# Kernel tuning notes

Hardware: AMD Instinct MI355X
Metric: run time of the kernel (lower is better)

The kernel has to match this reference:

```python
import jax, jax.numpy as jnp
import numpy as np

N, E, F, H, C, G = 100000, 800000, 128, 128, 10, 128
EPS = 1e-5


def setup_inputs() -> dict:
    key = jax.random.key(0)
    ks = jax.random.split(key, 8)
    return {
        "x": jax.random.normal(ks[0], (N, F), jnp.float32),
        "edge_index": jax.random.randint(ks[1], (2, E), 0, N),
        "batch": jnp.sort(jax.random.randint(ks[2], (N,), 0, G)),
        "edge_weight": jax.random.uniform(ks[3], (E,), jnp.float32, 0.1, 1.0),
        "bn_feat_w": jnp.ones((F,), jnp.float32),
        "bn_feat_b": jnp.full((F,), 1e-4, jnp.float32),
        "conv_feat_W": jax.random.normal(ks[4], (F, H), jnp.float32) / np.float32(np.sqrt(F)),
        "conv_feat_b": jnp.zeros((H,), jnp.float32),
        "bns_w": jnp.ones((3, H), jnp.float32),
        "bns_b": jnp.full((3, H), 1e-4, jnp.float32),
        "convs_W": jax.random.normal(ks[5], (3, H, H), jnp.float32) / np.float32(np.sqrt(H)),
        "convs_b": jnp.zeros((3, H), jnp.float32),
        "bn_fc_w": jnp.ones((H,), jnp.float32),
        "bn_fc_b": jnp.full((H,), 1e-4, jnp.float32),
        "lin_fc_W": jax.random.normal(ks[6], (H, H), jnp.float32) / np.float32(np.sqrt(H)),
        "lin_fc_b": jnp.zeros((H,), jnp.float32),
        "bn_hidden_w": jnp.ones((H,), jnp.float32),
        "bn_hidden_b": jnp.full((H,), 1e-4, jnp.float32),
        "lin_class_W": jax.random.normal(ks[7], (H, C), jnp.float32) / np.float32(np.sqrt(H)),
        "lin_class_b": jnp.zeros((C,), jnp.float32),
    }


def _bn(h, w, b):
    # training-mode BatchNorm1d: biased batch stats over dim 0
    mu = h.mean(0)
    var = jnp.mean((h - mu) ** 2, 0)
    return (h - mu) * jax.lax.rsqrt(var + EPS) * w + b


def reference(x, edge_index, batch, edge_weight,
              bn_feat_w, bn_feat_b, conv_feat_W, conv_feat_b,
              bns_w, bns_b, convs_W, convs_b,
              bn_fc_w, bn_fc_b, lin_fc_W, lin_fc_b,
              bn_hidden_w, bn_hidden_b, lin_class_W, lin_class_b):
    n = x.shape[0]
    loops = jnp.arange(n)
    # PyG GCNConv: add self-loops (weight 1) + symmetric normalization, shared by all convs
    row = jnp.concatenate([edge_index[0], loops])
    col = jnp.concatenate([edge_index[1], loops])
    ew = jnp.concatenate([edge_weight, jnp.ones((n,), x.dtype)])
    deg = jax.ops.segment_sum(ew, col, num_segments=n)
    dinv = jnp.where(deg > 0, jax.lax.rsqrt(jnp.maximum(deg, EPS)), 0.0)
    norm = (dinv[row] * ew * dinv[col])[:, None]  # [E+N, 1]

    def conv(h, W, b):
        m = (h @ W)[row] * norm                 # gather + scale per edge
        return jax.ops.segment_sum(m, col, num_segments=n) + b

    h = _bn(x, bn_feat_w, bn_feat_b)
    h = jax.nn.relu(conv(h, conv_feat_W, conv_feat_b))
    h_init = h

    x_list = []
    # branch 1: BN -> Conv -> ReLU chain
    h = h_init
    for i in range(3):
        h = jax.nn.relu(conv(_bn(h, bns_w[i], bns_b[i]), convs_W[i], convs_b[i]))
    x_list.append(h)
    # branch 2: double application of the same BN/Conv per step
    h = h_init
    for i in range(3):
        h_ = jax.nn.relu(conv(_bn(h, bns_w[i], bns_b[i]), convs_W[i], convs_b[i]))
        h = jax.nn.relu(conv(_bn(h_, bns_w[i], bns_b[i]), convs_W[i], convs_b[i]))
    x_list.append(h)
    # branch 3: identical to branch 1 when conv_residual=False
    h = h_init
    for i in range(3):
        h = jax.nn.relu(conv(_bn(h, bns_w[i], bns_b[i]), convs_W[i], convs_b[i]))
    x_list.append(h)
    # branch 4: BN -> ReLU only
    h = h_init
    for i in range(3):
        h = jax.nn.relu(_bn(h, bns_w[i], bns_b[i]))
    x_list.append(h)

    def head(hn):
        g = jax.ops.segment_sum(hn, batch, num_segments=G)  # global_add_pool
        g = jax.nn.relu(_bn(g, bn_fc_w, bn_fc_b) @ lin_fc_W + lin_fc_b)
        g = _bn(g, bn_hidden_w, bn_hidden_b)
        return jax.nn.log_softmax(g @ lin_class_W + lin_class_b, axis=-1)

    return tuple(head(hn) for hn in x_list)
```

## Files before the change

kernel.cpp:

```cpp
#include <hip/hip_runtime.h>

#define N_NODES 100000
#define NPAD    100032
#define NBLK    1563
#define NEDGE   800000
#define NGRP    128
#define NSLOT   32
#define EPS     1e-5f

typedef unsigned int   u32;
typedef unsigned short u16;
typedef short bf16x8 __attribute__((ext_vector_type(8)));
typedef float f32x4  __attribute__((ext_vector_type(4)));

__device__ __forceinline__ float bf2f(u32 u){ return __uint_as_float(u << 16); }
__device__ __forceinline__ u16 f2bf(float f){
  u32 x = __float_as_uint(f);
  x += 0x7fffu + ((x >> 16) & 1u);
  return (u16)(x >> 16);
}

__global__ void k_init(float* deg, int* cnt, int* fill, float* gbuf){
  int i = blockIdx.x * 256 + threadIdx.x;
  if (i < NPAD){ deg[i] = 1.0f; cnt[i] = 0; fill[i] = 0; }
  if (i < 4 * NGRP * 128) gbuf[i] = 0.f;
}

__global__ void k_deg(const int* __restrict__ col, const float* __restrict__ ew,
                      float* __restrict__ deg, int* __restrict__ cnt){
  int e = blockIdx.x * 256 + threadIdx.x;
  if (e < NEDGE){
    int c = col[e];
    atomicAdd(&deg[c], ew[e]);
    atomicAdd(&cnt[c], 1);
  }
}

__global__ void k_dinv(const float* __restrict__ deg, float* __restrict__ dinv, float* __restrict__ srow){
  int i = blockIdx.x * 256 + threadIdx.x;
  if (i < N_NODES){
    float d = deg[i];
    float v = d > 0.f ? rsqrtf(fmaxf(d, EPS)) : 0.f;
    dinv[i] = v; srow[i] = v * v;
  }
}

__global__ __launch_bounds__(256) void k_chunksum(const int* __restrict__ cnt, int* __restrict__ csum){
  int b = blockIdx.x, t = threadIdx.x;
  int s = 0;
  for (int i = t; i < 1024; i += 256){ int idx = b * 1024 + i; if (idx < N_NODES) s += cnt[idx]; }
  __shared__ int red[256];
  red[t] = s; __syncthreads();
  for (int o = 128; o > 0; o >>= 1){ if (t < o) red[t] += red[t + o]; __syncthreads(); }
  if (t == 0) csum[b] = red[0];
}

__global__ __launch_bounds__(128) void k_chunkscan(const int* __restrict__ csum, int* __restrict__ coff,
                                                   int* __restrict__ ptrA){
  int t = threadIdx.x;
  __shared__ int s[128];
  int v = (t < 98) ? csum[t] : 0;
  s[t] = v; __syncthreads();
  for (int o = 1; o < 128; o <<= 1){
    int x = (t >= o) ? s[t - o] : 0;
    __syncthreads(); s[t] += x; __syncthreads();
  }
  if (t < 98) coff[t] = s[t] - v;
  if (t == 0) ptrA[N_NODES] = NEDGE;
}

__global__ __launch_bounds__(256) void k_scan2(const int* __restrict__ cnt, const int* __restrict__ coff,
                                               int* __restrict__ ptrA){
  int b = blockIdx.x, t = threadIdx.x;
  int base = b * 1024 + t * 4;
  int v[4], tot = 0;
  #pragma unroll
  for (int k = 0; k < 4; k++){ int idx = base + k; v[k] = (idx < N_NODES) ? cnt[idx] : 0; tot += v[k]; }
  __shared__ int sc[256];
  sc[t] = tot; __syncthreads();
  for (int o = 1; o < 256; o <<= 1){
    int x = (t >= o) ? sc[t - o] : 0;
    __syncthreads(); sc[t] += x; __syncthreads();
  }
  int off = coff[b] + sc[t] - tot;
  #pragma unroll
  for (int k = 0; k < 4; k++){ int idx = base + k; if (idx < N_NODES) ptrA[idx] = off; off += v[k]; }
}

__global__ void k_fill(const int* __restrict__ row, const int* __restrict__ col,
                       const float* __restrict__ ew, const float* __restrict__ dinv,
                       const int* __restrict__ ptrA, int* __restrict__ fill, int2* __restrict__ adj,
                       float* __restrict__ srow){
  int e = blockIdx.x * 256 + threadIdx.x;
  if (e < NEDGE){
    int r = row[e], c = col[e];
    float w = dinv[r] * ew[e] * dinv[c];
    int pos = ptrA[c] + atomicAdd(&fill[c], 1);
    adj[pos] = make_int2(r, __float_as_int(w));
    atomicAdd(&srow[c], w);
  }
}

__global__ __launch_bounds__(256) void k_bhist(const int* __restrict__ batch, int* __restrict__ bpart){
  __shared__ int loc[128];
  int t = threadIdx.x;
  if (t < 128) loc[t] = 0;
  __syncthreads();
  int i = blockIdx.x * 256 + t;
  if (i < N_NODES) atomicAdd(&loc[batch[i]], 1);
  __syncthreads();
  if (t < 128) bpart[blockIdx.x * 128 + t] = loc[t];
}

__global__ __launch_bounds__(128) void k_bscan(const int* __restrict__ bpart, int* __restrict__ gptr){
  int t = threadIdx.x;
  int v = 0;
  for (int p = 0; p < 391; p++) v += bpart[p * 128 + t];
  __shared__ int s[128];
  s[t] = v; __syncthreads();
  for (int o = 1; o < 128; o <<= 1){
    int x = (t >= o) ? s[t - o] : 0;
    __syncthreads(); s[t] += x; __syncthreads();
  }
  gptr[t + 1] = s[t];
  if (t == 0) gptr[0] = 0;
}

__global__ __launch_bounds__(256) void k_cvtstats(const float* __restrict__ x, u32* __restrict__ dst,
                                                  float* __restrict__ sums_out){
  __shared__ float R[1024];
  int t = threadIdx.x;
  float s0 = 0.f, q0 = 0.f, s1 = 0.f, q1 = 0.f;
  size_t base = (size_t)blockIdx.x * 4096 + t;
  #pragma unroll
  for (int it = 0; it < 16; it++){
    size_t idx = base + (size_t)it * 256;
    if (idx < (size_t)N_NODES * 64){
      float2 v = ((const float2*)x)[idx];
      dst[idx] = (u32)f2bf(v.x) | ((u32)f2bf(v.y) << 16);
      s0 += v.x; q0 += v.x * v.x; s1 += v.y; q1 += v.y * v.y;
    }
  }
  R[t] = s0; R[256 + t] = q0; R[512 + t] = s1; R[768 + t] = q1;
  __syncthreads();
  if (t < 64){
    float S0 = 0.f, Q0 = 0.f, S1 = 0.f, Q1 = 0.f;
    #pragma unroll
    for (int g = 0; g < 4; g++){
      S0 += R[g * 64 + t];       Q0 += R[256 + g * 64 + t];
      S1 += R[512 + g * 64 + t]; Q1 += R[768 + g * 64 + t];
    }
    float* so = sums_out + (blockIdx.x & (NSLOT - 1)) * 256;
    atomicAdd(&so[2 * t], S0);
    atomicAdd(&so[2 * t + 1], S1);
    atomicAdd(&so[128 + 2 * t], Q0);
    atomicAdd(&so[128 + 2 * t + 1], Q1);
  }
}

__device__ __forceinline__ void fold_body(int blk, int t, const float* __restrict__ sums,
    const float* __restrict__ bw, const float* __restrict__ bb,
    const float* __restrict__ W, const float* __restrict__ bias,
    u16* __restrict__ Wh, u16* __restrict__ Wl, float* __restrict__ rb,
    float* scl, float* shf, float* stot, float* rred){
  {
    float s = 0.f;
    #pragma unroll 4
    for (int sl = 0; sl < NSLOT; sl++) s += sums[sl * 256 + t];
    stot[t] = s;
  }
  __syncthreads();
  if (t < 128){
    float mu  = stot[t] * (1.f / N_NODES);
    float var = stot[128 + t] * (1.f / N_NODES) - mu * mu;
    float sc  = bw[t] * rsqrtf(var + EPS);
    scl[t] = sc; shf[t] = bb[t] - mu * sc;
  }
  __syncthreads();
  {
    int idx = blk * 256 + t;
    int lane_ = idx & 63, sl = idx >> 6;
    int nt_ = sl >> 2, ks_ = sl & 3;
    int n_ = nt_ * 16 + (lane_ & 15);
    int kb = ks_ * 32 + (lane_ >> 4) * 8;
    u16 hi8[8], lo8[8];
    #pragma unroll
    for (int j = 0; j < 8; j++){
      float wv = W[(kb + j) * 128 + n_];
      float xv = scl[kb + j] * wv;
      u16 hh = f2bf(xv);
      hi8[j] = hh; lo8[j] = f2bf(xv - bf2f(hh));
    }
    uint4 ph, pl;
    ph.x = (u32)hi8[0] | ((u32)hi8[1] << 16); ph.y = (u32)hi8[2] | ((u32)hi8[3] << 16);
    ph.z = (u32)hi8[4] | ((u32)hi8[5] << 16); ph.w = (u32)hi8[6] | ((u32)hi8[7] << 16);
    pl.x = (u32)lo8[0] | ((u32)lo8[1] << 16); pl.y = (u32)lo8[2] | ((u32)lo8[3] << 16);
    pl.z = (u32)lo8[4] | ((u32)lo8[5] << 16); pl.w = (u32)lo8[6] | ((u32)lo8[7] << 16);
    *(uint4*)&Wh[idx * 8] = ph;
    *(uint4*)&Wl[idx * 8] = pl;
  }
  {
    int nl = t & 15, kk = t >> 4;
    int n2 = blk * 16 + nl;
    float rp = 0.f;
    #pragma unroll
    for (int j = 0; j < 8; j++){
      int k2 = kk * 8 + j;
      rp += shf[k2] * W[k2 * 128 + n2];
    }
    rred[t] = rp;
  }
  __syncthreads();
  if (t < 16){
    float s = 0.f;
    #pragma unroll
    for (int kk2 = 0; kk2 < 16; kk2++) s += rred[kk2 * 16 + t];
    int n2 = blk * 16 + t;
    rb[n2] = s;
    rb[128 + n2] = bias[n2];
  }
}

__global__ __launch_bounds__(256) void k_fold(const float* __restrict__ sums,
    const float* __restrict__ bw, const float* __restrict__ bb,
    const float* __restrict__ W, const float* __restrict__ bias,
    u16* __restrict__ Wh, u16* __restrict__ Wl, float* __restrict__ rb){
  __shared__ float scl[128], shf[128], stot[256], rred[256];
  fold_body(blockIdx.x, threadIdx.x, sums, bw, bb, W, bias, Wh, Wl, rb, scl, shf, stot, rred);
}

__global__ __launch_bounds__(256) void k_fold2(
    const float* __restrict__ sumsA, const float* __restrict__ bwA, const float* __restrict__ bbA,
    const float* __restrict__ WA, const float* __restrict__ biasA,
    u16* __restrict__ WhA, u16* __restrict__ WlA, float* __restrict__ rbA,
    const float* __restrict__ sumsB, const float* __restrict__ bwB, const float* __restrict__ bbB,
    const float* __restrict__ WB, const float* __restrict__ biasB,
    u16* __restrict__ WhB, u16* __restrict__ WlB, float* __restrict__ rbB){
  __shared__ float scl[128], shf[128], stot[256], rred[256];
  int bb_ = blockIdx.x;
  if (bb_ < 8)
    fold_body(bb_, threadIdx.x, sumsA, bwA, bbA, WA, biasA, WhA, WlA, rbA, scl, shf, stot, rred);
  else
    fold_body(bb_ - 8, threadIdx.x, sumsB, bwB, bbB, WB, biasB, WhB, WlB, rbB, scl, shf, stot, rred);
}

#define CONV_EPILOGUE(RB, HOUT, SOUT, BLK)                                     \
  __syncthreads();                                                             \
  sred[t] = 0.f;                                                               \
  __syncthreads();                                                             \
  _Pragma("unroll")                                                            \
  for (int nt = 0; nt < 8; nt++){                                              \
    int colc = nt * 16 + m;                                                    \
    float rv = RB[colc], bv = RB[128 + colc];                                  \
    float s = 0.f, qq = 0.f;                                                   \
    _Pragma("unroll")                                                          \
    for (int r = 0; r < 4; r++){                                               \
      int rown = row0 + q * 4 + r;                                             \
      float v = C[nt][r] + srow[rown] * rv + bv;                               \
      v = fmaxf(v, 0.f);                                                       \
      u16 sv = f2bf(v);                                                        \
      HOUT[(size_t)rown * 128 + colc] = sv;                                    \
      if (rown < N_NODES){ float vv = bf2f(sv); s += vv; qq += vv * vv; }      \
    }                                                                          \
    s  += __shfl_xor(s, 16, 64);  s  += __shfl_xor(s, 32, 64);                 \
    qq += __shfl_xor(qq, 16, 64); qq += __shfl_xor(qq, 32, 64);                \
    if (q == 0){                                                               \
      atomicAdd(&sred[colc], s);                                               \
      atomicAdd(&sred[128 + colc], qq);                                        \
    }                                                                          \
  }                                                                            \
  __syncthreads();                                                             \
  atomicAdd(&SOUT[((BLK) & (NSLOT - 1)) * 256 + t], sred[t]);

#define FMA_KS(KS, V, WT) \
  acc[KS][0] += (WT) * __uint_as_float((V).x << 16); acc[KS][1] += (WT) * __uint_as_float((V).x & 0xffff0000u); \
  acc[KS][2] += (WT) * __uint_as_float((V).y << 16); acc[KS][3] += (WT) * __uint_as_float((V).y & 0xffff0000u); \
  acc[KS][4] += (WT) * __uint_as_float((V).z << 16); acc[KS][5] += (WT) * __uint_as_float((V).z & 0xffff0000u); \
  acc[KS][6] += (WT) * __uint_as_float((V).w << 16); acc[KS][7] += (WT) * __uint_as_float((V).w & 0xffff0000u);

#define VMCNT_2()  asm volatile("s_waitcnt vmcnt(2)" ::: "memory")
#define VMCNT_6()  asm volatile("s_waitcnt vmcnt(6)" ::: "memory")
#define VMCNT_10() asm volatile("s_waitcnt vmcnt(10)" ::: "memory")
#define VMCNT_11() asm volatile("s_waitcnt vmcnt(11)" ::: "memory")

__device__ __forceinline__ void gll_stage(const u16* __restrict__ h, u16* dst, int2 aj, int lane){
  int c = lane & 15, g = lane >> 4;
  #pragma unroll
  for (int ii = 0; ii < 4; ii++){
    int rl = ii * 4 + g;
    int srcrow = __shfl(aj.x, rl, 64);
    const u16* src = h + (size_t)srcrow * 128 + (size_t)((c ^ rl) * 8);
    __builtin_amdgcn_global_load_lds((const void*)src, (void*)(dst + ii * 512), 16, 0, 0);
  }
}

#define GITER(WA_, WISS_, WD_, STG, J)                                         \
  WD_ = *(const int2*)(adj + base_ + min((J) + 5, dcl));                       \
  VMCNT_11();                                                                  \
  {                                                                            \
    float wgt = __int_as_float(__shfl((WA_).y, m, 64));                        \
    if ((J) < deg){                                                            \
      const u16* sp = stage + (STG) * 2048;                                    \
      _Pragma("unroll")                                                        \
      for (int ks = 0; ks < 4; ks++){                                          \
        int slot = (q + 4 * ks) ^ m;                                           \
        uint4 v = *(const uint4*)(sp + m * 128 + slot * 8);                    \
        FMA_KS(ks, v, wgt)                                                     \
      }                                                                        \
    }                                                                          \
  }                                                                            \
  VMCNT_10();                                                                  \
  gll_stage(h, stage + (STG) * 2048, WISS_, lane);

__device__ __forceinline__ void gather_row_lds(const u16* __restrict__ h,
    const int* __restrict__ ptrA, const int2* __restrict__ adj,
    const float* __restrict__ dinv, int row0, int lane, u16* stage,
    float (&acc)[4][8]){
  int m = lane & 15, q = lane >> 4;
  #pragma unroll
  for (int ks = 0; ks < 4; ks++)
    #pragma unroll
    for (int j = 0; j < 8; j++) acc[ks][j] = 0.f;
  int r = row0 + m;
  int r2 = min(r, N_NODES - 1);
  int b0 = ptrA[r2], b1 = ptrA[r2 + 1];
  int deg = (r < N_NODES) ? (b1 - b0) : 0;
  int base_ = min(b0, NEDGE - 1);
  int dcl = max(deg - 1, 0);
  float di = dinv[r2];
  float sw = (r < N_NODES) ? di * di : 0.f;
  const u16* hq = h + q * 8;
  const u16* sp_ = hq + (size_t)r2 * 128;
  uint4 s0 = *(const uint4*)(sp_);
  uint4 s1 = *(const uint4*)(sp_ + 32);
  uint4 s2 = *(const uint4*)(sp_ + 64);
  uint4 s3 = *(const uint4*)(sp_ + 96);
  int wmax = deg;
  wmax = max(wmax, __shfl_xor(wmax, 1, 64));
  wmax = max(wmax, __shfl_xor(wmax, 2, 64));
  wmax = max(wmax, __shfl_xor(wmax, 4, 64));
  wmax = max(wmax, __shfl_xor(wmax, 8, 64));
  FMA_KS(0, s0, sw) FMA_KS(1, s1, sw) FMA_KS(2, s2, sw) FMA_KS(3, s3, sw)
  if (wmax > 0){
    int2 W0 = *(const int2*)(adj + base_);
    int2 W1 = *(const int2*)(adj + base_ + min(1, dcl));
    int2 W2 = *(const int2*)(adj + base_ + min(2, dcl));
    int2 W3, W4, W5;
    VMCNT_2();
    gll_stage(h, stage, W0, lane);
    W3 = *(const int2*)(adj + base_ + min(3, dcl));
    VMCNT_6();
    gll_stage(h, stage + 2048, W1, lane);
    W4 = *(const int2*)(adj + base_ + min(4, dcl));
    VMCNT_10();
    gll_stage(h, stage + 4096, W2, lane);
    int j = 0;
    for (;;){
      GITER(W0, W3, W5, 0, j) if (++j >= wmax) break;
      GITER(W1, W4, W0, 1, j) if (++j >= wmax) break;
      GITER(W2, W5, W1, 2, j) if (++j >= wmax) break;
      GITER(W3, W0, W2, 0, j) if (++j >= wmax) break;
      GITER(W4, W1, W3, 1, j) if (++j >= wmax) break;
      GITER(W5, W2, W4, 2, j) if (++j >= wmax) break;
    }
  }
}

#define BUILD_AFRAG()                                                          \
  bf16x8 AH[4], AL[4];                                                         \
  _Pragma("unroll")                                                            \
  for (int ks = 0; ks < 4; ks++)                                               \
    _Pragma("unroll")                                                          \
    for (int j = 0; j < 8; j++){                                               \
      u16 hh = f2bf(acc[ks][j]);                                               \
      AH[ks][j] = (short)hh;                                                   \
      AL[ks][j] = (short)f2bf(acc[ks][j] - bf2f(hh));                          \
    }

#define MFMA_3PASS(WH, WL_)                                                    \
  _Pragma("unroll")                                                            \
  for (int ks = 0; ks < 4; ks++){                                              \
    _Pragma("unroll")                                                          \
    for (int nt = 0; nt < 8; nt++){                                            \
      bf16x8 bh = ((const bf16x8*)WH)[(nt * 4 + ks) * 64 + lane];              \
      bf16x8 bl = ((const bf16x8*)WL_)[(nt * 4 + ks) * 64 + lane];             \
      C[nt] = __builtin_amdgcn_mfma_f32_16x16x32_bf16(AH[ks], bh, C[nt], 0, 0, 0); \
      C[nt] = __builtin_amdgcn_mfma_f32_16x16x32_bf16(AL[ks], bh, C[nt], 0, 0, 0); \
      C[nt] = __builtin_amdgcn_mfma_f32_16x16x32_bf16(AH[ks], bl, C[nt], 0, 0, 0); \
    }                                                                          \
  }

__global__ __launch_bounds__(256, 3) void k_conv(
    const u16* __restrict__ h, const int* __restrict__ ptrA, const int2* __restrict__ adj,
    const float* __restrict__ dinv, const float* __restrict__ srow,
    const u16* __restrict__ Wh, const u16* __restrict__ Wl, const float* __restrict__ rb,
    u16* __restrict__ hout, float* __restrict__ sums_out){
  __shared__ u16 hstage[4][3][2048];
  __shared__ float sred[256];
  int t = threadIdx.x;
  int wave = t >> 6, lane = t & 63, m = lane & 15, q = lane >> 4;
  int blk = blockIdx.x;
  int row0 = blk * 64 + wave * 16;
  float acc[4][8];
  gather_row_lds(h, ptrA, adj, dinv, row0, lane, &hstage[wave][0][0], acc);
  BUILD_AFRAG()
  f32x4 C[8];
  #pragma unroll
  for (int nt = 0; nt < 8; nt++) C[nt] = f32x4{0.f, 0.f, 0.f, 0.f};
  MFMA_3PASS(Wh, Wl)
  CONV_EPILOGUE(rb, hout, sums_out, blk)
}

__global__ __launch_bounds__(256, 3) void k_conv2(
    const u16* __restrict__ hA, const u16* __restrict__ hB,
    const int* __restrict__ ptrA, const int2* __restrict__ adj,
    const float* __restrict__ dinv, const float* __restrict__ srow,
    const u16* __restrict__ WhA, const u16* __restrict__ WlA, const float* __restrict__ rbA,
    u16* __restrict__ houtA, float* __restrict__ sumsA,
    const u16* __restrict__ WhB, const u16* __restrict__ WlB, const float* __restrict__ rbB,
    u16* __restrict__ houtB, float* __restrict__ sumsB){
  __shared__ u16 hstage[4][3][2048];
  __shared__ float sred[256];
  int t = threadIdx.x;
  int wave = t >> 6, lane = t & 63, m = lane & 15, q = lane >> 4;
  int bb = blockIdx.x;
  int second = bb >= NBLK;
  int blk = second ? bb - NBLK : bb;
  const u16* h = second ? hB : hA;
  const u16* Wh = second ? WhB : WhA;
  const u16* Wl = second ? WlB : WlA;
  const float* rb = second ? rbB : rbA;
  u16* hout = second ? houtB : houtA;
  float* sums_out = second ? sumsB : sumsA;
  int row0 = blk * 64 + wave * 16;
  float acc[4][8];
  gather_row_lds(h, ptrA, adj, dinv, row0, lane, &hstage[wave][0][0], acc);
  BUILD_AFRAG()
  f32x4 C[8];
  #pragma unroll
  for (int nt = 0; nt < 8; nt++) C[nt] = f32x4{0.f, 0.f, 0.f, 0.f};
  MFMA_3PASS(Wh, Wl)
  CONV_EPILOGUE(rb, hout, sums_out, blk)
}

__global__ __launch_bounds__(256, 3) void k_dualconv(
    const u16* __restrict__ h, const int* __restrict__ ptrA, const int2* __restrict__ adj,
    const float* __restrict__ dinv, const float* __restrict__ srow,
    const u16* __restrict__ Wh1, const u16* __restrict__ Wl1, const float* __restrict__ rb1,
    u16* __restrict__ hout1, float* __restrict__ sums1,
    const u16* __restrict__ Wh2, const u16* __restrict__ Wl2, const float* __restrict__ rb2,
    u16* __restrict__ hout2, float* __restrict__ sums2){
  __shared__ u16 hstage[4][3][2048];
  __shared__ float sred[256];
  int t = threadIdx.x;
  int wave = t >> 6, lane = t & 63, m = lane & 15, q = lane >> 4;
  int blk = blockIdx.x;
  int row0 = blk * 64 + wave * 16;
  float acc[4][8];
  gather_row_lds(h, ptrA, adj, dinv, row0, lane, &hstage[wave][0][0], acc);
  BUILD_AFRAG()
  f32x4 C[8];
  #pragma unroll
  for (int nt = 0; nt < 8; nt++) C[nt] = f32x4{0.f, 0.f, 0.f, 0.f};
  MFMA_3PASS(Wh1, Wl1)
  CONV_EPILOGUE(rb1, hout1, sums1, blk)
  #pragma unroll
  for (int nt = 0; nt < 8; nt++) C[nt] = f32x4{0.f, 0.f, 0.f, 0.f};
  MFMA_3PASS(Wh2, Wl2)
  CONV_EPILOGUE(rb2, hout2, sums2, blk)
}

__global__ __launch_bounds__(256) void k_normrelu(const u16* __restrict__ h, const float* __restrict__ sums,
    const float* __restrict__ bw, const float* __restrict__ bb, u16* __restrict__ o,
    float* __restrict__ sums_out){
  __shared__ float scl[128], shf[128], R[2048], stot[256];
  int t = threadIdx.x;
  {
    float s = 0.f;
    #pragma unroll 4
    for (int sl = 0; sl < NSLOT; sl++) s += sums[sl * 256 + t];
    stot[t] = s;
  }
  __syncthreads();
  if (t < 128){
    float mu  = stot[t] * (1.f / N_NODES);
    float var = stot[128 + t] * (1.f / N_NODES) - mu * mu;
    float sc  = bw[t] * rsqrtf(var + EPS);
    scl[t] = sc; shf[t] = bb[t] - mu * sc;
  }
  __syncthreads();
  int c0 = (t & 31) * 4;
  float sc0 = scl[c0], sh0 = shf[c0], sc1 = scl[c0 + 1], sh1 = shf[c0 + 1];
  float sc2 = scl[c0 + 2], sh2 = shf[c0 + 2], sc3 = scl[c0 + 3], sh3 = shf[c0 + 3];
  float s0 = 0.f, q0 = 0.f, s1 = 0.f, q1 = 0.f, s2 = 0.f, q2 = 0.f, s3 = 0.f, q3 = 0.f;
  size_t base = (size_t)blockIdx.x * 2048 + t;
  #pragma unroll
  for (int it = 0; it < 8; it++){
    size_t idx = base + (size_t)it * 256;
    if (idx < (size_t)N_NODES * 32){
      uint2 v = ((const uint2*)h)[idx];
      float x0 = fmaxf(bf2f(v.x & 0xffffu) * sc0 + sh0, 0.f);
      float x1 = fmaxf(bf2f(v.x >> 16) * sc1 + sh1, 0.f);
      float x2 = fmaxf(bf2f(v.y & 0xffffu) * sc2 + sh2, 0.f);
      float x3 = fmaxf(bf2f(v.y >> 16) * sc3 + sh3, 0.f);
      u16 r0 = f2bf(x0), r1 = f2bf(x1), r2 = f2bf(x2), r3 = f2bf(x3);
      uint2 w;
      w.x = (u32)r0 | ((u32)r1 << 16);
      w.y = (u32)r2 | ((u32)r3 << 16);
      ((uint2*)o)[idx] = w;
      float y0 = bf2f(r0), y1 = bf2f(r1), y2 = bf2f(r2), y3 = bf2f(r3);
      s0 += y0; q0 += y0 * y0; s1 += y1; q1 += y1 * y1;
      s2 += y2; q2 += y2 * y2; s3 += y3; q3 += y3 * y3;
    }
  }
  R[t] = s0; R[256 + t] = s1; R[512 + t] = s2; R[768 + t] = s3;
  R[1024 + t] = q0; R[1280 + t] = q1; R[1536 + t] = q2; R[1792 + t] = q3;
  __syncthreads();
  if (t < 128){
    int j = t & 3, l = t >> 2;
    float S = 0.f, Q = 0.f;
    #pragma unroll
    for (int g = 0; g < 8; g++){
      int th = l + 32 * g;
      S += R[j * 256 + th];
      Q += R[1024 + j * 256 + th];
    }
    float* so = sums_out + (blockIdx.x & (NSLOT - 1)) * 256;
    atomicAdd(&so[t], S);
    atomicAdd(&so[128 + t], Q);
  }
}

__global__ __launch_bounds__(128) void k_pool(const u16* __restrict__ h, const int* __restrict__ gptr,
                                              float* __restrict__ gdst){
  __shared__ float part[2][16][8];
  int g = blockIdx.x >> 3, s = blockIdx.x & 7, t = threadIdx.x;
  int cc = t & 15, rr = t >> 4, wv = t >> 6, rrw = rr & 3;
  int b = gptr[g], e = gptr[g + 1];
  int len = e - b, per = (len + 7) >> 3;
  int r0 = b + s * per, r1 = min(r0 + per, e);
  float a[8] = {0.f, 0.f, 0.f, 0.f, 0.f, 0.f, 0.f, 0.f};
  for (int r = r0 + rr; r < r1; r += 8){
    uint4 v = *(const uint4*)(h + (size_t)r * 128 + cc * 8);
    a[0] += bf2f(v.x & 0xffffu); a[1] += bf2f(v.x >> 16);
    a[2] += bf2f(v.y & 0xffffu); a[3] += bf2f(v.y >> 16);
    a[4] += bf2f(v.z & 0xffffu); a[5] += bf2f(v.z >> 16);
    a[6] += bf2f(v.w & 0xffffu); a[7] += bf2f(v.w >> 16);
  }
  #pragma unroll
  for (int j = 0; j < 8; j++){
    a[j] += __shfl_xor(a[j], 16, 64);
    a[j] += __shfl_xor(a[j], 32, 64);
  }
  if (rrw == 0){
    #pragma unroll
    for (int j = 0; j < 8; j++) part[wv][cc][j] = a[j];
  }
  __syncthreads();
  {
    float sum = part[0][t >> 3][t & 7] + part[1][t >> 3][t & 7];
    atomicAdd(&gdst[g * 128 + t], sum);
  }
}

__global__ __launch_bounds__(256) void k_head(const float* __restrict__ gbuf,
    const float* __restrict__ fcw, const float* __restrict__ fcb,
    const float* __restrict__ Wfc, const float* __restrict__ bfc,
    const float* __restrict__ bhw, const float* __restrict__ bhb,
    const float* __restrict__ Wcl, const float* __restrict__ bcl,
    float* __restrict__ out){
  __shared__ float GS[128 * 65];
  __shared__ float ls[256], lq[256];
  __shared__ float scl[128], shf[128], scl2[128], shf2[128];
  __shared__ float sumT[128], sumQ[128];
  __shared__ float WclT[1280], Lrow[1280];
  int t = threadIdx.x, br = blockIdx.x;
  int slot = (br == 1) ? 1 : (br == 3 ? 3 : 0);
  const float* G = gbuf + slot * 16384;
  {
    int col = t & 127, hf2 = t >> 7;
    float s = 0.f, q = 0.f;
    for (int g = hf2 * 64; g < hf2 * 64 + 64; g++){ float v = G[g * 128 + col]; s += v; q += v * v; }
    ls[t] = s; lq[t] = q;
  }
  for (int idx = t; idx < 1280; idx += 256){
    int cc = idx >> 7, c = idx & 127;
    WclT[idx] = Wcl[c * 10 + cc];
  }
  if (t < 128){ sumT[t] = 0.f; sumQ[t] = 0.f; }
  __syncthreads();
  if (t < 128){
    float s = ls[t] + ls[t + 128], q = lq[t] + lq[t + 128];
    float mu = s * (1.f / 128), var = q * (1.f / 128) - mu * mu;
    float sc = fcw[t] * rsqrtf(var + EPS);
    scl[t] = sc; shf[t] = fcb[t] - mu * sc;
  }
  __syncthreads();
  int tr = t >> 4, tc = t & 15, r0 = tr * 8, c0 = tc * 8;
  float acc[8][8];
  #pragma unroll
  for (int a = 0; a < 8; a++)
    #pragma unroll
    for (int b = 0; b < 8; b++) acc[a][b] = 0.f;
  for (int kh = 0; kh < 2; kh++){
    for (int idx = t; idx < 8192; idx += 256){
      int r = idx >> 6, kk = idx & 63, f = kh * 64 + kk;
      GS[r * 65 + kk] = G[r * 128 + f] * scl[f] + shf[f];
    }
    __syncthreads();
    #pragma unroll 2
    for (int k = 0; k < 64; k++){
      float a[8];
      #pragma unroll
      for (int ri = 0; ri < 8; ri++) a[ri] = GS[(r0 + ri) * 65 + k];
      float4 b0 = *(const float4*)&Wfc[(kh * 64 + k) * 128 + c0];
      float4 b1 = *(const float4*)&Wfc[(kh * 64 + k) * 128 + c0 + 4];
      float bb[8] = {b0.x, b0.y, b0.z, b0.w, b1.x, b1.y, b1.z, b1.w};
      #pragma unroll
      for (int ri = 0; ri < 8; ri++)
        #pragma unroll
        for (int ci = 0; ci < 8; ci++) acc[ri][ci] += a[ri] * bb[ci];
    }
    __syncthreads();
  }
  #pragma unroll
  for (int ci = 0; ci < 8; ci++){
    float bb = bfc[c0 + ci];
    float s = 0.f, q = 0.f;
    #pragma unroll
    for (int ri = 0; ri < 8; ri++){
      float v = fmaxf(acc[ri][ci] + bb, 0.f);
      acc[ri][ci] = v; s += v; q += v * v;
    }
    atomicAdd(&sumT[c0 + ci], s);
    atomicAdd(&sumQ[c0 + ci], q);
  }
  __syncthreads();
  if (t < 128){
    float mu = sumT[t] * (1.f / 128), var = sumQ[t] * (1.f / 128) - mu * mu;
    float sc = bhw[t] * rsqrtf(var + EPS);
    scl2[t] = sc; shf2[t] = bhb[t] - mu * sc;
  }
  __syncthreads();
  #pragma unroll
  for (int ci = 0; ci < 8; ci++){
    float sc = scl2[c0 + ci], sh = shf2[c0 + ci];
    #pragma unroll
    for (int ri = 0; ri < 8; ri++) acc[ri][ci] = acc[ri][ci] * sc + sh;
  }
  #pragma unroll
  for (int ri = 0; ri < 8; ri++){
    float pl[10];
    #pragma unroll
    for (int cc = 0; cc < 10; cc++) pl[cc] = 0.f;
    #pragma unroll
    for (int ci = 0; ci < 8; ci++){
      float v = acc[ri][ci];
      #pragma unroll
      for (int cc = 0; cc < 10; cc++) pl[cc] += v * WclT[cc * 128 + c0 + ci];
    }
    #pragma unroll
    for (int msk = 1; msk < 16; msk <<= 1)
      #pragma unroll
      for (int cc = 0; cc < 10; cc++) pl[cc] += __shfl_xor(pl[cc], msk, 64);
    if (tc == 0)
      #pragma unroll
      for (int cc = 0; cc < 10; cc++) Lrow[(r0 + ri) * 10 + cc] = pl[cc];
  }
  __syncthreads();
  if (t < 128){
    float l[10];
    #pragma unroll
    for (int cc = 0; cc < 10; cc++) l[cc] = Lrow[t * 10 + cc] + bcl[cc];
    float m = l[0];
    #pragma unroll
    for (int cc = 1; cc < 10; cc++) m = fmaxf(m, l[cc]);
    float se = 0.f;
    #pragma unroll
    for (int cc = 0; cc < 10; cc++) se += expf(l[cc] - m);
    float lse = m + logf(se);
    #pragma unroll
    for (int cc = 0; cc < 10; cc++) out[br * 1280 + t * 10 + cc] = l[cc] - lse;
  }
}

extern "C" void kernel_launch(void* const* d_in, const int* in_sizes, int n_in,
                              void* d_out, int out_size, void* d_ws, size_t ws_size,
                              hipStream_t stream){
  const float* x    = (const float*)d_in[0];
  const int*  ei    = (const int*)d_in[1];
  const int*  batch = (const int*)d_in[2];
  const float* ew   = (const float*)d_in[3];
  const float* bnfw = (const float*)d_in[4];
  const float* bnfb = (const float*)d_in[5];
  const float* cfW  = (const float*)d_in[6];
  const float* cfb  = (const float*)d_in[7];
  const float* bnsw = (const float*)d_in[8];
  const float* bnsb = (const float*)d_in[9];
  const float* cvW  = (const float*)d_in[10];
  const float* cvb  = (const float*)d_in[11];
  const float* fcw  = (const float*)d_in[12];
  const float* fcb  = (const float*)d_in[13];
  const float* Wfc  = (const float*)d_in[14];
  const float* bfc  = (const float*)d_in[15];
  const float* bhw  = (const float*)d_in[16];
  const float* bhb  = (const float*)d_in[17];
  const float* Wcl  = (const float*)d_in[18];
  const float* bcl  = (const float*)d_in[19];
  float* out = (float*)d_out;

  char* p = (char*)d_ws;
  auto carve = [&](size_t bytes)->void*{ void* r = (void*)p; p += (bytes + 255) & ~(size_t)255; return r; };
  float* deg  = (float*)carve((size_t)NPAD * 4);
  float* dinv = (float*)carve((size_t)NPAD * 4);
  float* srow = (float*)carve((size_t)NPAD * 4);
  int*   cnt  = (int*)carve((size_t)NPAD * 4);
  int*   fill = (int*)carve((size_t)NPAD * 4);
  int*   ptrA = (int*)carve((size_t)(NPAD + 1) * 4);
  int*   bpart= (int*)carve((size_t)391 * 128 * 4);
  int*   csum = (int*)carve(512);
  int*   coff = (int*)carve(512);
  int*   gptr = (int*)carve(1024);
  float* S    = (float*)carve((size_t)13 * NSLOT * 1024);
  float* gbuf = (float*)carve(4 * 128 * 128 * 4);
  u16*   F0h  = (u16*)carve(32768);  u16* F0l = (u16*)carve(32768);  float* F0r = (float*)carve(1024);
  u16*   F1h  = (u16*)carve(32768);  u16* F1l = (u16*)carve(32768);  float* F1r = (float*)carve(1024);
  u16*   F2h  = (u16*)carve(32768);  u16* F2l = (u16*)carve(32768);  float* F2r = (float*)carve(1024);
  u16*   B0   = (u16*)carve((size_t)NPAD * 256);
  u16*   B1   = (u16*)carve((size_t)NPAD * 256);
  u16*   B2   = (u16*)carve((size_t)NPAD * 256);
  u16*   B3   = (u16*)carve((size_t)NPAD * 256);
  int2*  adj  = (int2*)carve((size_t)NEDGE * 8);
  u16*   Xb   = B3;
  auto Sb = [&](int i){ return S + (size_t)i * NSLOT * 256; };

  (void)hipMemsetAsync(S, 0, (size_t)13 * NSLOT * 1024, stream);

  k_init<<<392, 256, 0, stream>>>(deg, cnt, fill, gbuf);
  k_deg<<<3125, 256, 0, stream>>>(ei + NEDGE, ew, deg, cnt);
  k_dinv<<<391, 256, 0, stream>>>(deg, dinv, srow);
  k_chunksum<<<98, 256, 0, stream>>>(cnt, csum);
  k_chunkscan<<<1, 128, 0, stream>>>(csum, coff, ptrA);
  k_scan2<<<98, 256, 0, stream>>>(cnt, coff, ptrA);
  k_fill<<<3125, 256, 0, stream>>>(ei, ei + NEDGE, ew, dinv, ptrA, fill, adj, srow);
  k_bhist<<<391, 256, 0, stream>>>(batch, bpart);
  k_bscan<<<1, 128, 0, stream>>>(bpart, gptr);
  k_cvtstats<<<NBLK, 256, 0, stream>>>(x, (u32*)Xb, Sb(0));

  auto fold = [&](const float* Sin, const float* bw, const float* bb,
                  const float* W, const float* bias, u16* Fh, u16* Fl, float* Fr){
    k_fold<<<8, 256, 0, stream>>>(Sin, bw, bb, W, bias, Fh, Fl, Fr);
  };
  auto conv = [&](const u16* hin, const u16* Fh, const u16* Fl, const float* Fr,
                  u16* hout, float* Sout){
    k_conv<<<NBLK, 256, 0, stream>>>(hin, ptrA, adj, dinv, srow, Fh, Fl, Fr, hout, Sout);
  };

  fold(Sb(0), bnfw, bnfb, cfW, cfb, F0h, F0l, F0r);
  conv(Xb, F0h, F0l, F0r, B0, Sb(1));
  fold(Sb(1), bnsw, bnsb, cvW, cvb, F1h, F1l, F1r);
  conv(B0, F1h, F1l, F1r, B1, Sb(2));
  k_normrelu<<<NBLK, 256, 0, stream>>>(B0, Sb(1), bnsw,       bnsb,       B2, Sb(3));
  k_normrelu<<<NBLK, 256, 0, stream>>>(B2, Sb(3), bnsw + 128, bnsb + 128, B3, Sb(4));
  k_normrelu<<<NBLK, 256, 0, stream>>>(B3, Sb(4), bnsw + 256, bnsb + 256, B2, Sb(12));
  k_pool<<<1024, 128, 0, stream>>>(B2, gptr, gbuf + 3 * 16384);
  k_fold2<<<16, 256, 0, stream>>>(
      Sb(2), bnsw + 128, bnsb + 128, cvW + 16384, cvb + 128, F0h, F0l, F0r,
      Sb(2), bnsw,       bnsb,       cvW,         cvb,       F1h, F1l, F1r);
  k_dualconv<<<NBLK, 256, 0, stream>>>(B1, ptrA, adj, dinv, srow,
      F0h, F0l, F0r, B3, Sb(5),
      F1h, F1l, F1r, B2, Sb(6));
  k_fold2<<<16, 256, 0, stream>>>(
      Sb(5), bnsw + 256, bnsb + 256, cvW + 32768, cvb + 256, F2h, F2l, F2r,
      Sb(6), bnsw + 128, bnsb + 128, cvW + 16384, cvb + 128, F0h, F0l, F0r);
  k_conv2<<<2 * NBLK, 256, 0, stream>>>(B3, B2, ptrA, adj, dinv, srow,
      F2h, F2l, F2r, B0, Sb(10),
      F0h, F0l, F0r, B1, Sb(7));
  k_pool<<<1024, 128, 0, stream>>>(B0, gptr, gbuf);
  fold(Sb(7), bnsw + 128, bnsb + 128, cvW + 16384, cvb + 128, F1h, F1l, F1r);
  conv(B1, F1h, F1l, F1r, B2, Sb(8));
  fold(Sb(8), bnsw + 256, bnsb + 256, cvW + 32768, cvb + 256, F2h, F2l, F2r);
  conv(B2, F2h, F2l, F2r, B1, Sb(9));
  fold(Sb(9), bnsw + 256, bnsb + 256, cvW + 32768, cvb + 256, F0h, F0l, F0r);
  conv(B1, F0h, F0l, F0r, B3, Sb(11));
  k_pool<<<1024, 128, 0, stream>>>(B3, gptr, gbuf + 16384);

  k_head<<<4, 256, 0, stream>>>(gbuf, fcw, fcb, Wfc, bfc, bhw, bhb, Wcl, bcl, out);
}
```

Measured before the change: 1.056 ms.

## Shrink gather pipeline to two LDS stages and raise occupancy to four blocks

Reworks the neighbour-gather software pipeline from three LDS staging buffers (adjacency prefetch five ahead) to two buffers (prefetch three ahead). Wait counts are retuned to match and sched_barriers pin the instruction order. The first two adjacency loads are hoisted before the degree reduction. Launch bounds go from 3 to 4 blocks per CU, using the freed LDS and registers to hide gather latency with more waves in place of deeper per-wave prefetch. The risk is more exposed latency per wave, and fragile hand-set vmcnt values that could break correctness if the load count is off.

```diff
diff --git a/kernel.cpp b/kernel.cpp
--- a/kernel.cpp
+++ b/kernel.cpp
@@ -278,10 +278,9 @@
   acc[KS][4] += (WT) * __uint_as_float((V).z << 16); acc[KS][5] += (WT) * __uint_as_float((V).z & 0xffff0000u); \
   acc[KS][6] += (WT) * __uint_as_float((V).w << 16); acc[KS][7] += (WT) * __uint_as_float((V).w & 0xffff0000u);
 
-#define VMCNT_2()  asm volatile("s_waitcnt vmcnt(2)" ::: "memory")
-#define VMCNT_6()  asm volatile("s_waitcnt vmcnt(6)" ::: "memory")
-#define VMCNT_10() asm volatile("s_waitcnt vmcnt(10)" ::: "memory")
-#define VMCNT_11() asm volatile("s_waitcnt vmcnt(11)" ::: "memory")
+#define VMCNT6() asm volatile("s_waitcnt vmcnt(6)" ::: "memory")
+#define VMCNT5() asm volatile("s_waitcnt vmcnt(5)" ::: "memory")
+#define SB0()    __builtin_amdgcn_sched_barrier(0)
 
 __device__ __forceinline__ void gll_stage(const u16* __restrict__ h, u16* dst, int2 aj, int lane){
   int c = lane & 15, g = lane >> 4;
@@ -294,11 +293,11 @@
   }
 }
 
-#define GITER(WA_, WISS_, WD_, STG, J)                                         \
-  WD_ = *(const int2*)(adj + base_ + min((J) + 5, dcl));                       \
-  VMCNT_11();                                                                  \
+#define GITER(WA, WB, WC, WD, STG, J)                                          \
+  WD = *(const int2*)(adj + base_ + min((J) + 3, dcl));                        \
+  VMCNT6();                                                                    \
   {                                                                            \
-    float wgt = __int_as_float(__shfl((WA_).y, m, 64));                        \
+    float wgt = __int_as_float(__shfl((WA).y, m, 64));                         \
     if ((J) < deg){                                                            \
       const u16* sp = stage + (STG) * 2048;                                    \
       _Pragma("unroll")                                                        \
@@ -309,8 +308,9 @@
       }                                                                        \
     }                                                                          \
   }                                                                            \
-  VMCNT_10();                                                                  \
-  gll_stage(h, stage + (STG) * 2048, WISS_, lane);
+  VMCNT5();                                                                    \
+  gll_stage(h, stage + (STG) * 2048, WC, lane);                                \
+  SB0();
 
 __device__ __forceinline__ void gather_row_lds(const u16* __restrict__ h,
     const int* __restrict__ ptrA, const int2* __restrict__ adj,
@@ -335,6 +335,8 @@
   uint4 s1 = *(const uint4*)(sp_ + 32);
   uint4 s2 = *(const uint4*)(sp_ + 64);
   uint4 s3 = *(const uint4*)(sp_ + 96);
+  int2 W0 = *(const int2*)(adj + base_);
+  int2 W1 = *(const int2*)(adj + base_ + min(1, dcl));
   int wmax = deg;
   wmax = max(wmax, __shfl_xor(wmax, 1, 64));
   wmax = max(wmax, __shfl_xor(wmax, 2, 64));
@@ -342,26 +344,22 @@
   wmax = max(wmax, __shfl_xor(wmax, 8, 64));
   FMA_KS(0, s0, sw) FMA_KS(1, s1, sw) FMA_KS(2, s2, sw) FMA_KS(3, s3, sw)
   if (wmax > 0){
-    int2 W0 = *(const int2*)(adj + base_);
-    int2 W1 = *(const int2*)(adj + base_ + min(1, dcl));
-    int2 W2 = *(const int2*)(adj + base_ + min(2, dcl));
-    int2 W3, W4, W5;
-    VMCNT_2();
+    int2 W2 = W0, W3 = W0;
+    SB0();
     gll_stage(h, stage, W0, lane);
-    W3 = *(const int2*)(adj + base_ + min(3, dcl));
-    VMCNT_6();
+    SB0();
+    W2 = *(const int2*)(adj + base_ + min(2, dcl));
+    SB0();
     gll_stage(h, stage + 2048, W1, lane);
-    W4 = *(const int2*)(adj + base_ + min(4, dcl));
-    VMCNT_10();
-    gll_stage(h, stage + 4096, W2, lane);
-    int j = 0;
+    SB0();
+    int j0 = 0;
     for (;;){
-      GITER(W0, W3, W5, 0, j) if (++j >= wmax) break;
-      GITER(W1, W4, W0, 1, j) if (++j >= wmax) break;
-      GITER(W2, W5, W1, 2, j) if (++j >= wmax) break;
-      GITER(W3, W0, W2, 0, j) if (++j >= wmax) break;
-      GITER(W4, W1, W3, 1, j) if (++j >= wmax) break;
-      GITER(W5, W2, W4, 2, j) if (++j >= wmax) break;
+      GITER(W0, W1, W2, W3, 0, j0)
+      GITER(W1, W2, W3, W0, 1, j0 + 1)
+      j0 += 2; if (j0 >= wmax) break;
+      GITER(W2, W3, W0, W1, 0, j0)
+      GITER(W3, W0, W1, W2, 1, j0 + 1)
+      j0 += 2; if (j0 >= wmax) break;
     }
   }
 }
@@ -390,12 +388,12 @@
     }                                                                          \
   }
 
-__global__ __launch_bounds__(256, 3) void k_conv(
+__global__ __launch_bounds__(256, 4) void k_conv(
     const u16* __restrict__ h, const int* __restrict__ ptrA, const int2* __restrict__ adj,
     const float* __restrict__ dinv, const float* __restrict__ srow,
     const u16* __restrict__ Wh, const u16* __restrict__ Wl, const float* __restrict__ rb,
     u16* __restrict__ hout, float* __restrict__ sums_out){
-  __shared__ u16 hstage[4][3][2048];
+  __shared__ u16 hstage[4][2][2048];
   __shared__ float sred[256];
   int t = threadIdx.x;
   int wave = t >> 6, lane = t & 63, m = lane & 15, q = lane >> 4;
@@ -411,7 +409,7 @@
   CONV_EPILOGUE(rb, hout, sums_out, blk)
 }
 
-__global__ __launch_bounds__(256, 3) void k_conv2(
+__global__ __launch_bounds__(256, 4) void k_conv2(
     const u16* __restrict__ hA, const u16* __restrict__ hB,
     const int* __restrict__ ptrA, const int2* __restrict__ adj,
     const float* __restrict__ dinv, const float* __restrict__ srow,
@@ -419,7 +417,7 @@
     u16* __restrict__ houtA, float* __restrict__ sumsA,
     const u16* __restrict__ WhB, const u16* __restrict__ WlB, const float* __restrict__ rbB,
     u16* __restrict__ houtB, float* __restrict__ sumsB){
-  __shared__ u16 hstage[4][3][2048];
+  __shared__ u16 hstage[4][2][2048];
   __shared__ float sred[256];
   int t = threadIdx.x;
   int wave = t >> 6, lane = t & 63, m = lane & 15, q = lane >> 4;
@@ -443,14 +441,14 @@
   CONV_EPILOGUE(rb, hout, sums_out, blk)
 }
 
-__global__ __launch_bounds__(256, 3) void k_dualconv(
+__global__ __launch_bounds__(256, 4) void k_dualconv(
     const u16* __restrict__ h, const int* __restrict__ ptrA, const int2* __restrict__ adj,
     const float* __restrict__ dinv, const float* __restrict__ srow,
     const u16* __restrict__ Wh1, const u16* __restrict__ Wl1, const float* __restrict__ rb1,
     u16* __restrict__ hout1, float* __restrict__ sums1,
     const u16* __restrict__ Wh2, const u16* __restrict__ Wl2, const float* __restrict__ rb2,
     u16* __restrict__ hout2, float* __restrict__ sums2){
-  __shared__ u16 hstage[4][3][2048];
+  __shared__ u16 hstage[4][2][2048];
   __shared__ float sred[256];
   int t = threadIdx.x;
   int wave = t >> 6, lane = t & 63, m = lane & 15, q = lane >> 4;
```

Measured after the change: 990.5 us (median of 2 runs). 6.2% less time.
